# Kernel optimization log

Measured on AMD Instinct MI355X. Metric: run time of the kernel, lower is better.

## Reference

```python
import jax, jax.numpy as jnp
import numpy as np


def _index3d(pts, R):
    # voxel-grid lookup: floor(p * R) per axis, clipped into the grid, flattened
    idx = jnp.clip(jnp.floor(pts * R).astype(jnp.int32), 0, R - 1)
    return (idx[:, 0] * R + idx[:, 1]) * R + idx[:, 2]


def _dist_count(pts_t, closest_points, mask, R, weight=1.0):
    # gather closest surface point per voxel, masked L2 distance, mean-reduce
    idx = _index3d(pts_t, R)
    closest = jnp.take(closest_points, idx, axis=0)  # [N,3]
    dist = jnp.sqrt(jnp.sum((pts_t - closest) ** 2, axis=1))  # [N]
    return jnp.mean(dist * jnp.take(mask, idx)) * weight


def _qmul(q, r):
    # Hamilton product, broadcasting over leading dims
    w1, x1, y1, z1 = q[..., 0], q[..., 1], q[..., 2], q[..., 3]
    w2, x2, y2, z2 = r[..., 0], r[..., 1], r[..., 2], r[..., 3]
    return jnp.stack([
        w1 * w2 - x1 * x2 - y1 * y2 - z1 * z2,
        w1 * x2 + x1 * w2 + y1 * z2 - z1 * y2,
        w1 * y2 - x1 * z2 + y1 * w2 + z1 * x2,
        w1 * z2 + x1 * y2 - y1 * x2 + z1 * w2,
    ], axis=-1)


def setup_inputs() -> dict:
    key = jax.random.key(0)
    k1, k2, k3, k4, k5 = jax.random.split(key, 5)
    N = 4_194_304  # sample points
    R = 64         # voxel grid resolution
    return {
        "sample_points": jax.random.uniform(k1, (N, 3), dtype=jnp.float32),
        "closest_points": jax.random.uniform(k2, (R ** 3, 3), dtype=jnp.float32),
        "voxels": jax.random.randint(k3, (R ** 3,), 0, 2, dtype=jnp.int32),
        "planes": jax.random.normal(k4, (3, 4), dtype=jnp.float32),
        "axes": jax.random.normal(k5, (3, 4), dtype=jnp.float32),
        "resolution": R,
    }


def reference(sample_points, closest_points, voxels, planes, axes, resolution):
    R = resolution
    mask = voxels.astype(sample_points.dtype)  # [R^3] occupancy mask

    def reflect_one(plane):
        n, d = plane[:3], plane[3]
        # p' = p - 2 n (p.n + d) / (n.n)
        coef = 2.0 * (sample_points @ n + d) / jnp.dot(n, n)  # [N]
        pts_t = sample_points - coef[:, None] * n
        return _dist_count(pts_t, closest_points, mask, R)

    def rotate_one(quat):
        zeros = jnp.zeros((sample_points.shape[0], 1), sample_points.dtype)
        p4 = jnp.concatenate([zeros, sample_points], axis=1)  # pure quaternion [N,4]
        q_inv = quat * jnp.array([1.0, -1.0, -1.0, -1.0], quat.dtype)
        pts_t = _qmul(_qmul(quat[None, :], p4), q_inv[None, :])[:, 1:]  # q * p * q^-1
        return _dist_count(pts_t, closest_points, mask, R)

    reflect_loss = jnp.sum(jax.vmap(reflect_one)(planes))
    rotate_loss = jnp.sum(jax.vmap(rotate_one)(axes))
    return reflect_loss + rotate_loss
```

## Files before the change

### kernel.cpp

```cpp
#include <hip/hip_runtime.h>
#include <stdint.h>

#define RES 64
#define NVOX (RES * RES * RES)
#define NPTS 4194304
#define TPB 256
#define MAIN_BLOCKS 2048


__global__ __launch_bounds__(256) void build_table_kernel(
    const float* __restrict__ cp, const int* __restrict__ vox,
    uint32_t* __restrict__ tq)
{
    int i = blockIdx.x * 256 + threadIdx.x;
    float x = cp[3 * i + 0];
    float y = cp[3 * i + 1];
    float z = cp[3 * i + 2];
    uint32_t qx = (uint32_t)__float2int_rn(fminf(fmaxf(x, 0.f), 1.f) * 1023.0f);
    uint32_t qy = (uint32_t)__float2int_rn(fminf(fmaxf(y, 0.f), 1.f) * 1023.0f);
    uint32_t qz = (uint32_t)__float2int_rn(fminf(fmaxf(z, 0.f), 1.f) * 1023.0f);
    uint32_t m  = (vox[i] != 0) ? (1u << 30) : 0u;
    tq[i] = qx | (qy << 10) | (qz << 20) | m;
}

__device__ __forceinline__ int voxel_index(float x, float y, float z)
{
    float fx = __builtin_amdgcn_fmed3f(floorf(x * 64.0f), 0.0f, 63.0f);
    float fy = __builtin_amdgcn_fmed3f(floorf(y * 64.0f), 0.0f, 63.0f);
    float fz = __builtin_amdgcn_fmed3f(floorf(z * 64.0f), 0.0f, 63.0f);
    int ix = (int)fx, iy = (int)fy, iz = (int)fz;
    return (ix << 12) | (iy << 6) | iz;
}

__global__ __launch_bounds__(256) void sym_loss_kernel(
    const float4* __restrict__ pts,
    const float* __restrict__ planes,
    const float* __restrict__ axes,
    const uint32_t* __restrict__ tq,
    float* __restrict__ out)
{
    const int tid = threadIdx.x;

    float nx[3], ny[3], nz[3], nd[3], nsc[3];
#pragma unroll
    for (int k = 0; k < 3; ++k) {
        float a = planes[4 * k + 0], b = planes[4 * k + 1];
        float c = planes[4 * k + 2], d = planes[4 * k + 3];
        nx[k] = a; ny[k] = b; nz[k] = c; nd[k] = d;
        nsc[k] = 2.0f / (a * a + b * b + c * c);
    }
    float qs[3], qvx[3], qvy[3], qvz[3], q2w[3];
#pragma unroll
    for (int k = 0; k < 3; ++k) {
        float w = axes[4 * k + 0], x = axes[4 * k + 1];
        float y = axes[4 * k + 2], z = axes[4 * k + 3];
        qs[k]  = w * w - (x * x + y * y + z * z);
        qvx[k] = x; qvy[k] = y; qvz[k] = z;
        q2w[k] = 2.0f * w;
    }

    const int gid    = blockIdx.x * TPB + tid;
    const int stride = MAIN_BLOCKS * TPB;

    float acc = 0.0f;
#pragma unroll
    for (int g = 0; g < 2; ++g) {
        int base = gid + g * stride;
        float4 f0 = pts[3 * base + 0];
        float4 f1 = pts[3 * base + 1];
        float4 f2 = pts[3 * base + 2];
        float px[4] = {f0.x, f0.w, f1.z, f2.y};
        float py[4] = {f0.y, f1.x, f1.w, f2.z};
        float pz[4] = {f0.z, f1.y, f2.x, f2.w};

#pragma unroll
        for (int j = 0; j < 4; ++j) {
            float x = px[j], y = py[j], z = pz[j];
            float tx[6], ty[6], tz[6];

#pragma unroll
            for (int k = 0; k < 3; ++k) {
                float coef = (x * nx[k] + y * ny[k] + z * nz[k] + nd[k]) * nsc[k];
                tx[k] = x - coef * nx[k];
                ty[k] = y - coef * ny[k];
                tz[k] = z - coef * nz[k];
            }
#pragma unroll
            for (int k = 0; k < 3; ++k) {
                float dot2 = 2.0f * (qvx[k] * x + qvy[k] * y + qvz[k] * z);
                float cx = qvy[k] * z - qvz[k] * y;
                float cy = qvz[k] * x - qvx[k] * z;
                float cz = qvx[k] * y - qvy[k] * x;
                tx[3 + k] = qs[k] * x + dot2 * qvx[k] + q2w[k] * cx;
                ty[3 + k] = qs[k] * y + dot2 * qvy[k] + q2w[k] * cy;
                tz[3 + k] = qs[k] * z + dot2 * qvz[k] + q2w[k] * cz;
            }

            uint32_t e[6];
#pragma unroll
            for (int t = 0; t < 6; ++t)
                e[t] = tq[voxel_index(tx[t], ty[t], tz[t])];

#pragma unroll
            for (int t = 0; t < 6; ++t) {
                uint32_t w = e[t];
                float cx = (float)(w & 1023u)         * (1.0f / 1023.0f);
                float cy = (float)((w >> 10) & 1023u) * (1.0f / 1023.0f);
                float cz = (float)((w >> 20) & 1023u) * (1.0f / 1023.0f);
                float dx = tx[t] - cx, dy = ty[t] - cy, dz = tz[t] - cz;
                float d2 = dx * dx + dy * dy + dz * dz;
                float m  = (float)(w >> 30);
                acc += sqrtf(d2) * m;
            }
        }
    }

#pragma unroll
    for (int off = 32; off > 0; off >>= 1)
        acc += __shfl_down(acc, off, 64);

    __shared__ float sacc[4];
    int lane = tid & 63;
    int wid  = tid >> 6;
    if (lane == 0) sacc[wid] = acc;
    __syncthreads();
    if (tid == 0) {
        float s = sacc[0] + sacc[1] + sacc[2] + sacc[3];
        atomicAdd(out, s * (1.0f / (float)NPTS));
    }
}

extern "C" void kernel_launch(void* const* d_in, const int* in_sizes, int n_in,
                              void* d_out, int out_size, void* d_ws, size_t ws_size,
                              hipStream_t stream)
{
    const float* sample_points = (const float*)d_in[0];
    const float* closest       = (const float*)d_in[1];
    const int*   voxels        = (const int*)d_in[2];
    const float* planes        = (const float*)d_in[3];
    const float* axes          = (const float*)d_in[4];
    float*       out           = (float*)d_out;

    uint32_t* tq = (uint32_t*)d_ws;

    (void)hipMemsetAsync(out, 0, sizeof(float), stream);
    build_table_kernel<<<NVOX / 256, 256, 0, stream>>>(closest, voxels, tq);
    sym_loss_kernel<<<MAIN_BLOCKS, TPB, 0, stream>>>(
        (const float4*)sample_points, planes, axes, tq, out);
}
```

Baseline: 157.5 us.

## Stage occupancy bitmask in LDS and redirect empty-voxel gathers to one entry

The build kernel now also writes a 1-bit-per-voxel occupancy bitmask (32 KB). Every block of the main kernel copies it into shared memory and tests occupancy there, so lookups for empty voxels are sent to entry 0 of the table instead of scattered addresses. This is meant to cut random global gather traffic roughly in half. In exchange, every block pays a 32 KB LDS fill, which also limits occupancy. Block size doubles to 512 and the grid shrinks to match, keeping 8 points per thread.

```diff
diff --git a/kernel.cpp b/kernel.cpp
--- a/kernel.cpp
+++ b/kernel.cpp
@@ -4,13 +4,13 @@
 #define RES 64
 #define NVOX (RES * RES * RES)
 #define NPTS 4194304
-#define TPB 256
-#define MAIN_BLOCKS 2048
+#define TPB 512
+#define MAIN_BLOCKS (NPTS / 8 / TPB)
 
 
 __global__ __launch_bounds__(256) void build_table_kernel(
     const float* __restrict__ cp, const int* __restrict__ vox,
-    uint32_t* __restrict__ tq)
+    uint32_t* __restrict__ tq, unsigned long long* __restrict__ mbits)
 {
     int i = blockIdx.x * 256 + threadIdx.x;
     float x = cp[3 * i + 0];
@@ -21,6 +21,9 @@
     uint32_t qz = (uint32_t)__float2int_rn(fminf(fmaxf(z, 0.f), 1.f) * 1023.0f);
     uint32_t m  = (vox[i] != 0) ? (1u << 30) : 0u;
     tq[i] = qx | (qy << 10) | (qz << 20) | m;
+
+    unsigned long long b = __ballot(vox[i] != 0);
+    if ((threadIdx.x & 63) == 0) mbits[i >> 6] = b;
 }
 
 __device__ __forceinline__ int voxel_index(float x, float y, float z)
@@ -32,14 +35,21 @@
     return (ix << 12) | (iy << 6) | iz;
 }
 
-__global__ __launch_bounds__(256) void sym_loss_kernel(
+__global__ __launch_bounds__(TPB, 8) void sym_loss_kernel(
     const float4* __restrict__ pts,
     const float* __restrict__ planes,
     const float* __restrict__ axes,
     const uint32_t* __restrict__ tq,
+    const uint32_t* __restrict__ mbits,
     float* __restrict__ out)
 {
+    __shared__ uint32_t smask[NVOX / 32];
+    __shared__ float sacc[TPB / 64];
+
     const int tid = threadIdx.x;
+#pragma unroll
+    for (int i = 0; i < NVOX / 32 / TPB; ++i)
+        smask[i * TPB + tid] = mbits[i * TPB + tid];
 
     float nx[3], ny[3], nz[3], nd[3], nsc[3];
 #pragma unroll
@@ -58,6 +68,8 @@
         qvx[k] = x; qvy[k] = y; qvz[k] = z;
         q2w[k] = 2.0f * w;
     }
+
+    __syncthreads();
 
     const int gid    = blockIdx.x * TPB + tid;
     const int stride = MAIN_BLOCKS * TPB;
@@ -97,9 +109,14 @@
             }
 
             uint32_t e[6];
+            float    mm[6];
 #pragma unroll
-            for (int t = 0; t < 6; ++t)
-                e[t] = tq[voxel_index(tx[t], ty[t], tz[t])];
+            for (int t = 0; t < 6; ++t) {
+                int idx = voxel_index(tx[t], ty[t], tz[t]);
+                uint32_t bit = (smask[idx >> 5] >> (idx & 31)) & 1u;
+                mm[t] = (float)bit;
+                e[t]  = tq[bit ? idx : 0];
+            }
 
 #pragma unroll
             for (int t = 0; t < 6; ++t) {
@@ -108,9 +125,7 @@
                 float cy = (float)((w >> 10) & 1023u) * (1.0f / 1023.0f);
                 float cz = (float)((w >> 20) & 1023u) * (1.0f / 1023.0f);
                 float dx = tx[t] - cx, dy = ty[t] - cy, dz = tz[t] - cz;
-                float d2 = dx * dx + dy * dy + dz * dz;
-                float m  = (float)(w >> 30);
-                acc += sqrtf(d2) * m;
+                acc += sqrtf(dx * dx + dy * dy + dz * dz) * mm[t];
             }
         }
     }
@@ -119,13 +134,14 @@
     for (int off = 32; off > 0; off >>= 1)
         acc += __shfl_down(acc, off, 64);
 
-    __shared__ float sacc[4];
     int lane = tid & 63;
     int wid  = tid >> 6;
     if (lane == 0) sacc[wid] = acc;
     __syncthreads();
     if (tid == 0) {
-        float s = sacc[0] + sacc[1] + sacc[2] + sacc[3];
+        float s = 0.0f;
+#pragma unroll
+        for (int wv = 0; wv < TPB / 64; ++wv) s += sacc[wv];
         atomicAdd(out, s * (1.0f / (float)NPTS));
     }
 }
@@ -141,10 +157,12 @@
     const float* axes          = (const float*)d_in[4];
     float*       out           = (float*)d_out;
 
-    uint32_t* tq = (uint32_t*)d_ws;
+    uint32_t*           tq    = (uint32_t*)d_ws;
+    unsigned long long* mbits = (unsigned long long*)((char*)d_ws + NVOX * 4);
 
     (void)hipMemsetAsync(out, 0, sizeof(float), stream);
-    build_table_kernel<<<NVOX / 256, 256, 0, stream>>>(closest, voxels, tq);
+    build_table_kernel<<<NVOX / 256, 256, 0, stream>>>(closest, voxels, tq, mbits);
     sym_loss_kernel<<<MAIN_BLOCKS, TPB, 0, stream>>>(
-        (const float4*)sample_points, planes, axes, tq, out);
+        (const float4*)sample_points, planes, axes, tq,
+        (const uint32_t*)mbits, out);
 }
```

New measurement: 131.5 us. -16.5%, faster.
